# Performance work log

Hardware: AMD Instinct MI355X
Metric: run time of the kernel (lower is better)

## Reference

```python
import jax, jax.numpy as jnp
import numpy as np

EPS = 1e-6
K_HOPS = 2  # SGConv K


def setup_inputs() -> dict:
    key = jax.random.key(0)
    k1, k2, k3, k4 = jax.random.split(key, 4)
    B, Kk, C, T = 32, 8, 64, 250
    E, H = 4096, 128
    x = jax.random.normal(k1, (B, Kk, C, T), dtype=jnp.float32)
    edge_index = jax.random.randint(k2, (2, E), 0, C, dtype=jnp.int64)
    edge_weights = jax.random.uniform(k3, (E,), dtype=jnp.float32)
    W = jax.random.normal(k4, (H, Kk * T), dtype=jnp.float32) * 0.02
    b = jnp.zeros((H,), dtype=jnp.float32)
    return {"x": x, "edge_index": edge_index, "edge_weights": edge_weights, "W": W, "b": b}


def reference(x, edge_index, edge_weights, W, b):
    B, Kk, C, T = x.shape
    N = C  # nodes
    x = x.reshape(B, N, Kk * T)  # (B, N, F)

    # clamp non-positive edge weights to epsilon (mirrors in-place .data clamp)
    w = jnp.where(edge_weights <= 0, EPS, edge_weights)

    # gcn_norm with self loops (fill value 1.0)
    src, dst = edge_index[0], edge_index[1]
    loop = jnp.arange(N, dtype=edge_index.dtype)
    src = jnp.concatenate([src, loop])
    dst = jnp.concatenate([dst, loop])
    w = jnp.concatenate([w, jnp.ones((N,), w.dtype)])
    deg = jnp.zeros((N,), w.dtype).at[dst].add(w)
    dinv = jnp.where(deg > 0, deg ** -0.5, jnp.zeros_like(deg))
    norm = dinv[src] * w * dinv[dst]  # (E+N,)

    # K hops of gather -> weight -> scatter-add aggregation
    for _ in range(K_HOPS):
        msg = x[:, src, :] * norm[None, :, None]        # (B, E+N, F)
        x = jnp.zeros_like(x).at[:, dst, :].add(msg)    # (B, N, F)

    # final linear: y = x @ W^T + b
    return jnp.einsum('bnf,hf->bnh', x, W) + b
```

## Files before the change

kernel.cpp:

```cpp
#include <hip/hip_runtime.h>
#include <hip/hip_bf16.h>

#define EPSW 1e-6f

typedef __attribute__((ext_vector_type(4))) float floatx4;
typedef __attribute__((ext_vector_type(8))) short shortx8;

__device__ __forceinline__ unsigned short f2bf(float f) {
    unsigned int u = __float_as_uint(f);
    u = (u + 0x7fffu + ((u >> 16) & 1u)) >> 16;
    return (unsigned short)u;
}

__global__ __launch_bounds__(256) void prep(const float* __restrict__ x,
                                            const float* __restrict__ W,
                                            const int* __restrict__ ei,
                                            const float* __restrict__ ew,
                                            unsigned short* __restrict__ xt,
                                            unsigned short* __restrict__ wt,
                                            float* __restrict__ Mt) {
    __shared__ __align__(16) unsigned char smem[64 * 264 * 2];
    const int bid = blockIdx.x;
    const int t   = threadIdx.x;

    if (bid < 256) {
        unsigned short(*tile)[264] = (unsigned short(*)[264])smem;
        const int rb   = (bid >> 3) * 64;
        const int kgb  = (bid & 7) * 32;
        const int kbas = kgb * 8;
#pragma unroll
        for (int i = 0; i < 16; ++i) {
            const int idx = i * 256 + t;
            const int r   = idx >> 6;
            const int kc  = (idx & 63) * 4;
            const int k   = kbas + kc;
            floatx4 v = (floatx4){0.f, 0.f, 0.f, 0.f};
            if (k < 2000)
                v = *(const floatx4*)(x + (size_t)(rb + r) * 2000 + k);
            tile[r][kc + 0] = f2bf(v.x);
            tile[r][kc + 1] = f2bf(v.y);
            tile[r][kc + 2] = f2bf(v.z);
            tile[r][kc + 3] = f2bf(v.w);
        }
        __syncthreads();
#pragma unroll
        for (int i = 0; i < 8; ++i) {
            const int kg_l = i * 4 + (t >> 6);
            const int r    = t & 63;
            const shortx8 g = *(const shortx8*)&tile[r][kg_l * 8];
            *(shortx8*)(xt + ((size_t)(kgb + kg_l) * 2048 + rb + r) * 8) = g;
        }
    } else if (bid < 272) {
#pragma unroll
        for (int i = 0; i < 8; ++i) {
            const int G  = (bid - 256) * 2048 + i * 256 + t;
            const int kg = G >> 7;
            const int h  = G & 127;
            const int k  = kg * 8;
            floatx4 v0 = (floatx4){0.f, 0.f, 0.f, 0.f};
            floatx4 v1 = (floatx4){0.f, 0.f, 0.f, 0.f};
            if (k < 2000) {
                v0 = *(const floatx4*)(W + (size_t)h * 2000 + k);
                v1 = *(const floatx4*)(W + (size_t)h * 2000 + k + 4);
            }
            unsigned short* p = wt + ((size_t)kg * 128 + h) * 8;
            p[0] = f2bf(v0.x); p[1] = f2bf(v0.y); p[2] = f2bf(v0.z); p[3] = f2bf(v0.w);
            p[4] = f2bf(v1.x); p[5] = f2bf(v1.y); p[6] = f2bf(v1.z); p[7] = f2bf(v1.w);
        }
    } else {
        float* A    = (float*)smem;
        float* deg  = (float*)(smem + 16384);
        float* dinv = deg + 64;
        if (t < 64) deg[t] = 1.0f;
        for (int i = t; i < 4096; i += 256) A[i] = 0.0f;
        __syncthreads();
        const int* src = ei;
        const int* dst = ei + 4096;
        for (int e = t; e < 4096; e += 256) {
            float w = ew[e];
            w = (w <= 0.0f) ? EPSW : w;
            atomicAdd(&deg[dst[e]], w);
        }
        __syncthreads();
        if (t < 64) dinv[t] = 1.0f / sqrtf(deg[t]);
        __syncthreads();
        for (int e = t; e < 4096; e += 256) {
            float w = ew[e];
            w = (w <= 0.0f) ? EPSW : w;
            const int s = src[e], d = dst[e];
            atomicAdd(&A[d * 64 + s], dinv[s] * w * dinv[d]);
        }
        if (t < 64) atomicAdd(&A[t * 64 + t], dinv[t] * dinv[t]);
        __syncthreads();
#pragma unroll
        for (int i = 0; i < 16; ++i) {
            const int idx = i * 256 + t;
            const int n = idx >> 6, c = idx & 63;
            float s = 0.0f;
#pragma unroll 8
            for (int k = 0; k < 64; ++k) s += A[n * 64 + k] * A[k * 64 + c];
            Mt[c * 64 + n] = s;
        }
    }
}

__global__ __launch_bounds__(512) void gemm_apply(
        const unsigned short* __restrict__ xt,
        const unsigned short* __restrict__ wt,
        const float* __restrict__ Mt,
        const float* __restrict__ bias,
        float* __restrict__ y) {
    __shared__ float Ms[4096];
    __shared__ float zs[64][17];
    const int t    = threadIdx.x;
    const int wave = t >> 6, lane = t & 63;
    const int m = lane & 15, q = lane >> 4;
    const int ht = blockIdx.x;
    const int b  = blockIdx.y;
    const int rt = wave & 3, kh = wave >> 2;

    {
        const floatx4* Mg4 = (const floatx4*)Mt;
        floatx4* Ms4 = (floatx4*)Ms;
        Ms4[t]       = Mg4[t];
        Ms4[t + 512] = Mg4[t + 512];
    }

    const shortx8* Ag = (const shortx8*)xt;
    const shortx8* Bg = (const shortx8*)wt;
    int ga = (kh * 128 + q) * 2048 + b * 64 + rt * 16 + m;
    int gb = (kh * 128 + q) * 128 + ht * 16 + m;

    floatx4 acc0 = (floatx4){0.f, 0.f, 0.f, 0.f};
    floatx4 acc1 = (floatx4){0.f, 0.f, 0.f, 0.f};
#pragma unroll 4
    for (int kt = 0; kt < 32; kt += 2) {
        const shortx8 a0 = Ag[ga];
        const shortx8 b0 = Bg[gb];
        const shortx8 a1 = Ag[ga + 8192];
        const shortx8 b1 = Bg[gb + 512];
        acc0 = __builtin_amdgcn_mfma_f32_16x16x32_bf16(a0, b0, acc0, 0, 0, 0);
        acc1 = __builtin_amdgcn_mfma_f32_16x16x32_bf16(a1, b1, acc1, 0, 0, 0);
        ga += 16384; gb += 1024;
    }
    acc0 += acc1;

    __syncthreads();
    if (kh == 0) {
#pragma unroll
        for (int v = 0; v < 4; ++v) zs[rt * 16 + q * 4 + v][m] = acc0[v];
    }
    __syncthreads();
    if (kh == 1) {
#pragma unroll
        for (int v = 0; v < 4; ++v) zs[rt * 16 + q * 4 + v][m] += acc0[v];
    }
    __syncthreads();

    {
        const int n0 = t >> 4;
        const int h  = t & 15;
        const float bv = bias[ht * 16 + h];
        float s0 = bv, s1 = bv;
#pragma unroll
        for (int mm = 0; mm < 64; ++mm) {
            const float zv = zs[mm][h];
            s0 += Ms[mm * 64 + n0]      * zv;
            s1 += Ms[mm * 64 + n0 + 32] * zv;
        }
        float* yp = y + (size_t)b * 8192 + ht * 16 + h;
        yp[(size_t)n0 * 128]        = s0;
        yp[(size_t)(n0 + 32) * 128] = s1;
    }
}

extern "C" void kernel_launch(void* const* d_in, const int* in_sizes, int n_in,
                              void* d_out, int out_size, void* d_ws, size_t ws_size,
                              hipStream_t stream) {
    const float* x    = (const float*)d_in[0];
    const int*   ei   = (const int*)d_in[1];
    const float* ew   = (const float*)d_in[2];
    const float* W    = (const float*)d_in[3];
    const float* bias = (const float*)d_in[4];
    float* y = (float*)d_out;

    float* Mt = (float*)d_ws;
    unsigned short* xt = (unsigned short*)(Mt + 4096);
    unsigned short* wt = xt + 4194304;

    prep<<<273, 256, 0, stream>>>(x, W, ei, ew, xt, wt, Mt);
    gemm_apply<<<dim3(8, 32), 512, 0, stream>>>(xt, wt, Mt, bias, y);
}
```

Before: 102.5 us.

## Fuse prep and GEMM kernels into one launch with global counter spin-waits

Merges the bf16 conversion/transposition, graph-propagation matrix build and GEMM-apply kernels into a single 256-block kernel. Cross-block dependencies are handled with atomic counters in the workspace and spin-waits with sleep. The propagation matrix is computed by 16 blocks in parallel, and its wait is deferred until after the MFMA loop so that work can overlap. This removes a kernel launch and its boundary, but it needs all blocks to be co-resident. It also assumes the counter memory starts at either 0 or a 0xAA fill pattern, and the counters are never reset between calls.

```diff
diff --git a/kernel.cpp b/kernel.cpp
--- a/kernel.cpp
+++ b/kernel.cpp
@@ -2,6 +2,7 @@
 #include <hip/hip_bf16.h>
 
 #define EPSW 1e-6f
+#define BASEP 0xAAAAAAAAu
 
 typedef __attribute__((ext_vector_type(4))) float floatx4;
 typedef __attribute__((ext_vector_type(8))) short shortx8;
@@ -12,25 +13,34 @@
     return (unsigned short)u;
 }
 
-__global__ __launch_bounds__(256) void prep(const float* __restrict__ x,
-                                            const float* __restrict__ W,
-                                            const int* __restrict__ ei,
-                                            const float* __restrict__ ew,
-                                            unsigned short* __restrict__ xt,
-                                            unsigned short* __restrict__ wt,
-                                            float* __restrict__ Mt) {
-    __shared__ __align__(16) unsigned char smem[64 * 264 * 2];
+__device__ __forceinline__ void spin_until(const unsigned int* p, unsigned int tgt) {
+    for (int i = 0; i < 1000000; ++i) {
+        const unsigned int v =
+            __hip_atomic_load(p, __ATOMIC_RELAXED, __HIP_MEMORY_SCOPE_AGENT);
+        if (v == tgt || v == tgt + BASEP) return;
+        __builtin_amdgcn_s_sleep(2);
+    }
+}
+
+__global__ __launch_bounds__(512, 2) void fused(
+        const float* __restrict__ x, const float* __restrict__ W,
+        const int* __restrict__ ei, const float* __restrict__ ew,
+        const float* __restrict__ bias,
+        unsigned short* __restrict__ xt, unsigned short* __restrict__ wt,
+        float* __restrict__ Mt, unsigned int* __restrict__ ctr,
+        float* __restrict__ y) {
+    __shared__ __align__(16) unsigned char smem[50688];
     const int bid = blockIdx.x;
     const int t   = threadIdx.x;
 
-    if (bid < 256) {
+    {
         unsigned short(*tile)[264] = (unsigned short(*)[264])smem;
         const int rb   = (bid >> 3) * 64;
         const int kgb  = (bid & 7) * 32;
         const int kbas = kgb * 8;
 #pragma unroll
-        for (int i = 0; i < 16; ++i) {
-            const int idx = i * 256 + t;
+        for (int i = 0; i < 8; ++i) {
+            const int idx = i * 512 + t;
             const int r   = idx >> 6;
             const int kc  = (idx & 63) * 4;
             const int k   = kbas + kc;
@@ -44,17 +54,19 @@
         }
         __syncthreads();
 #pragma unroll
-        for (int i = 0; i < 8; ++i) {
-            const int kg_l = i * 4 + (t >> 6);
+        for (int i = 0; i < 4; ++i) {
+            const int kg_l = i * 8 + (t >> 6);
             const int r    = t & 63;
             const shortx8 g = *(const shortx8*)&tile[r][kg_l * 8];
             *(shortx8*)(xt + ((size_t)(kgb + kg_l) * 2048 + rb + r) * 8) = g;
         }
-    } else if (bid < 272) {
-#pragma unroll
-        for (int i = 0; i < 8; ++i) {
-            const int G  = (bid - 256) * 2048 + i * 256 + t;
-            const int kg = G >> 7;
+    }
+
+    if (bid < 16) {
+#pragma unroll
+        for (int i = 0; i < 4; ++i) {
+            const int G  = i * 512 + t;
+            const int kg = bid * 16 + (G >> 7);
             const int h  = G & 127;
             const int k  = kg * 8;
             floatx4 v0 = (floatx4){0.f, 0.f, 0.f, 0.f};
@@ -67,64 +79,65 @@
             p[0] = f2bf(v0.x); p[1] = f2bf(v0.y); p[2] = f2bf(v0.z); p[3] = f2bf(v0.w);
             p[4] = f2bf(v1.x); p[5] = f2bf(v1.y); p[6] = f2bf(v1.z); p[7] = f2bf(v1.w);
         }
-    } else {
-        float* A    = (float*)smem;
-        float* deg  = (float*)(smem + 16384);
-        float* dinv = deg + 64;
+    }
+
+    __syncthreads();
+    __threadfence();
+    if (t == 0) {
+        atomicAdd(&ctr[bid >> 3], 1u);
+        if (bid < 16) atomicAdd(&ctr[32], 1u);
+    }
+
+    if (bid >= 240) {
+        float* A    = (float*)(smem + 33792);
+        float* deg  = (float*)(smem + 50176);
+        float* dinv = (float*)(smem + 50432);
         if (t < 64) deg[t] = 1.0f;
-        for (int i = t; i < 4096; i += 256) A[i] = 0.0f;
-        __syncthreads();
-        const int* src = ei;
-        const int* dst = ei + 4096;
-        for (int e = t; e < 4096; e += 256) {
+        for (int i = t; i < 4096; i += 512) A[i] = 0.0f;
+        __syncthreads();
+        const int* srcp = ei;
+        const int* dstp = ei + 4096;
+        for (int e = t; e < 4096; e += 512) {
             float w = ew[e];
             w = (w <= 0.0f) ? EPSW : w;
-            atomicAdd(&deg[dst[e]], w);
+            atomicAdd(&deg[dstp[e]], w);
         }
         __syncthreads();
         if (t < 64) dinv[t] = 1.0f / sqrtf(deg[t]);
         __syncthreads();
-        for (int e = t; e < 4096; e += 256) {
+        for (int e = t; e < 4096; e += 512) {
             float w = ew[e];
             w = (w <= 0.0f) ? EPSW : w;
-            const int s = src[e], d = dst[e];
+            const int s = srcp[e], d = dstp[e];
             atomicAdd(&A[d * 64 + s], dinv[s] * w * dinv[d]);
         }
         if (t < 64) atomicAdd(&A[t * 64 + t], dinv[t] * dinv[t]);
         __syncthreads();
-#pragma unroll
-        for (int i = 0; i < 16; ++i) {
-            const int idx = i * 256 + t;
-            const int n = idx >> 6, c = idx & 63;
+        if (t < 256) {
+            const int c = (bid - 240) * 4 + (t >> 6);
+            const int n = t & 63;
             float s = 0.0f;
 #pragma unroll 8
             for (int k = 0; k < 64; ++k) s += A[n * 64 + k] * A[k * 64 + c];
             Mt[c * 64 + n] = s;
         }
-    }
-}
-
-__global__ __launch_bounds__(512) void gemm_apply(
-        const unsigned short* __restrict__ xt,
-        const unsigned short* __restrict__ wt,
-        const float* __restrict__ Mt,
-        const float* __restrict__ bias,
-        float* __restrict__ y) {
-    __shared__ float Ms[4096];
-    __shared__ float zs[64][17];
-    const int t    = threadIdx.x;
+        __syncthreads();
+        __threadfence();
+        if (t == 0) atomicAdd(&ctr[33], 1u);
+    }
+
+    const int b  = bid >> 3;
+    const int ht = bid & 7;
+    if (t == 0) {
+        spin_until(&ctr[b], 8u);
+        spin_until(&ctr[32], 16u);
+    }
+    __syncthreads();
+    __threadfence();
+
     const int wave = t >> 6, lane = t & 63;
     const int m = lane & 15, q = lane >> 4;
-    const int ht = blockIdx.x;
-    const int b  = blockIdx.y;
     const int rt = wave & 3, kh = wave >> 2;
-
-    {
-        const floatx4* Mg4 = (const floatx4*)Mt;
-        floatx4* Ms4 = (floatx4*)Ms;
-        Ms4[t]       = Mg4[t];
-        Ms4[t + 512] = Mg4[t + 512];
-    }
 
     const shortx8* Ag = (const shortx8*)xt;
     const shortx8* Bg = (const shortx8*)wt;
@@ -145,7 +158,18 @@
     }
     acc0 += acc1;
 
-    __syncthreads();
+    if (t == 0) spin_until(&ctr[33], 16u);
+    __syncthreads();
+    __threadfence();
+
+    float* Ms      = (float*)smem;
+    float(*zs)[17] = (float(*)[17])(smem + 16384);
+    {
+        const floatx4* Mg4 = (const floatx4*)Mt;
+        floatx4* Ms4 = (floatx4*)Ms;
+        Ms4[t]       = Mg4[t];
+        Ms4[t + 512] = Mg4[t + 512];
+    }
     if (kh == 0) {
 #pragma unroll
         for (int v = 0; v < 4; ++v) zs[rt * 16 + q * 4 + v][m] = acc0[v];
@@ -156,7 +180,6 @@
         for (int v = 0; v < 4; ++v) zs[rt * 16 + q * 4 + v][m] += acc0[v];
     }
     __syncthreads();
-
     {
         const int n0 = t >> 4;
         const int h  = t & 15;
@@ -187,7 +210,7 @@
     float* Mt = (float*)d_ws;
     unsigned short* xt = (unsigned short*)(Mt + 4096);
     unsigned short* wt = xt + 4194304;
-
-    prep<<<273, 256, 0, stream>>>(x, W, ei, ew, xt, wt, Mt);
-    gemm_apply<<<dim3(8, 32), 512, 0, stream>>>(xt, wt, Mt, bias, y);
-}
+    unsigned int* ctr  = (unsigned int*)(wt + 262144);
+
+    fused<<<256, 512, 0, stream>>>(x, W, ei, ew, bias, xt, wt, Mt, ctr, y);
+}
```

Measured after the change: 212.6 us. +107.5%, slower.

## Fuse prep and GEMM into one kernel with in-block bf16 conversion and LDS staging

Applied to the files above, without the earlier changes.

Merges the conversion/propagation-matrix prep kernel and the GEMM-apply kernel into a single launch. Each block recomputes the 64x64 two-hop propagation matrix in LDS, then streams fp32 x and W chunks from global memory, converts them to bf16 in registers with a cheaper perm-based pack, and stages them in double-buffered LDS for MFMA. This removes the second launch and the global round trip through bf16 workspace copies. In exchange every block redundantly builds the graph matrix with atomics and an O(64^3) product, x is re-read by all 8 head tiles, and the rounding drops the round-to-even tie handling.

```diff
diff --git a/kernel.cpp b/kernel.cpp
--- a/kernel.cpp
+++ b/kernel.cpp
@@ -6,146 +6,134 @@
 typedef __attribute__((ext_vector_type(4))) float floatx4;
 typedef __attribute__((ext_vector_type(8))) short shortx8;
 
-__device__ __forceinline__ unsigned short f2bf(float f) {
-    unsigned int u = __float_as_uint(f);
-    u = (u + 0x7fffu + ((u >> 16) & 1u)) >> 16;
-    return (unsigned short)u;
+__device__ __forceinline__ shortx8 pack8(floatx4 a, floatx4 b) {
+    union { shortx8 v; unsigned int u[4]; } r;
+    const unsigned a0 = __float_as_uint(a.x) + 0x8000u, a1 = __float_as_uint(a.y) + 0x8000u;
+    const unsigned a2 = __float_as_uint(a.z) + 0x8000u, a3 = __float_as_uint(a.w) + 0x8000u;
+    const unsigned b0 = __float_as_uint(b.x) + 0x8000u, b1 = __float_as_uint(b.y) + 0x8000u;
+    const unsigned b2 = __float_as_uint(b.z) + 0x8000u, b3 = __float_as_uint(b.w) + 0x8000u;
+    r.u[0] = __builtin_amdgcn_perm(a1, a0, 0x07060302u);
+    r.u[1] = __builtin_amdgcn_perm(a3, a2, 0x07060302u);
+    r.u[2] = __builtin_amdgcn_perm(b1, b0, 0x07060302u);
+    r.u[3] = __builtin_amdgcn_perm(b3, b2, 0x07060302u);
+    return r.v;
 }
 
-__global__ __launch_bounds__(256) void prep(const float* __restrict__ x,
-                                            const float* __restrict__ W,
-                                            const int* __restrict__ ei,
-                                            const float* __restrict__ ew,
-                                            unsigned short* __restrict__ xt,
-                                            unsigned short* __restrict__ wt,
-                                            float* __restrict__ Mt) {
-    __shared__ __align__(16) unsigned char smem[64 * 264 * 2];
+#define XSTR 136
+
+__global__ __launch_bounds__(512, 2) void fused_all(
+        const float* __restrict__ x, const float* __restrict__ W,
+        const int* __restrict__ ei, const float* __restrict__ ew,
+        const float* __restrict__ bias, float* __restrict__ y) {
+    __shared__ __align__(16) unsigned short smem[29952];
+    unsigned short* xs0 = smem;
+    unsigned short* xs1 = smem + 8704;
+    unsigned short* ww0 = smem + 17408;
+    unsigned short* ww1 = smem + 19584;
+    float* Ms = (float*)(smem + 21760);
+    float* A    = (float*)smem;
+    float* deg  = (float*)xs1;
+    float* dinv = deg + 64;
+    float(*zs)[17] = (float(*)[17])smem;
+
+    const int t   = threadIdx.x;
     const int bid = blockIdx.x;
-    const int t   = threadIdx.x;
+    const int b   = bid & 31;
+    const int ht  = bid >> 5;
 
-    if (bid < 256) {
-        unsigned short(*tile)[264] = (unsigned short(*)[264])smem;
-        const int rb   = (bid >> 3) * 64;
-        const int kgb  = (bid & 7) * 32;
-        const int kbas = kgb * 8;
-#pragma unroll
-        for (int i = 0; i < 16; ++i) {
-            const int idx = i * 256 + t;
-            const int r   = idx >> 6;
-            const int kc  = (idx & 63) * 4;
-            const int k   = kbas + kc;
-            floatx4 v = (floatx4){0.f, 0.f, 0.f, 0.f};
-            if (k < 2000)
-                v = *(const floatx4*)(x + (size_t)(rb + r) * 2000 + k);
-            tile[r][kc + 0] = f2bf(v.x);
-            tile[r][kc + 1] = f2bf(v.y);
-            tile[r][kc + 2] = f2bf(v.z);
-            tile[r][kc + 3] = f2bf(v.w);
-        }
+    {
+        if (t < 64) deg[t] = 1.0f;
+        for (int i = t; i < 4096; i += 512) A[i] = 0.0f;
         __syncthreads();
+        const int* srcp = ei;
+        const int* dstp = ei + 4096;
 #pragma unroll
         for (int i = 0; i < 8; ++i) {
-            const int kg_l = i * 4 + (t >> 6);
-            const int r    = t & 63;
-            const shortx8 g = *(const shortx8*)&tile[r][kg_l * 8];
-            *(shortx8*)(xt + ((size_t)(kgb + kg_l) * 2048 + rb + r) * 8) = g;
-        }
-    } else if (bid < 272) {
-#pragma unroll
-        for (int i = 0; i < 8; ++i) {
-            const int G  = (bid - 256) * 2048 + i * 256 + t;
-            const int kg = G >> 7;
-            const int h  = G & 127;
-            const int k  = kg * 8;
-            floatx4 v0 = (floatx4){0.f, 0.f, 0.f, 0.f};
-            floatx4 v1 = (floatx4){0.f, 0.f, 0.f, 0.f};
-            if (k < 2000) {
-                v0 = *(const floatx4*)(W + (size_t)h * 2000 + k);
-                v1 = *(const floatx4*)(W + (size_t)h * 2000 + k + 4);
-            }
-            unsigned short* p = wt + ((size_t)kg * 128 + h) * 8;
-            p[0] = f2bf(v0.x); p[1] = f2bf(v0.y); p[2] = f2bf(v0.z); p[3] = f2bf(v0.w);
-            p[4] = f2bf(v1.x); p[5] = f2bf(v1.y); p[6] = f2bf(v1.z); p[7] = f2bf(v1.w);
-        }
-    } else {
-        float* A    = (float*)smem;
-        float* deg  = (float*)(smem + 16384);
-        float* dinv = deg + 64;
-        if (t < 64) deg[t] = 1.0f;
-        for (int i = t; i < 4096; i += 256) A[i] = 0.0f;
-        __syncthreads();
-        const int* src = ei;
-        const int* dst = ei + 4096;
-        for (int e = t; e < 4096; e += 256) {
+            const int e = i * 512 + t;
             float w = ew[e];
             w = (w <= 0.0f) ? EPSW : w;
-            atomicAdd(&deg[dst[e]], w);
+            atomicAdd(&deg[dstp[e]], w);
         }
         __syncthreads();
         if (t < 64) dinv[t] = 1.0f / sqrtf(deg[t]);
         __syncthreads();
-        for (int e = t; e < 4096; e += 256) {
+#pragma unroll
+        for (int i = 0; i < 8; ++i) {
+            const int e = i * 512 + t;
             float w = ew[e];
             w = (w <= 0.0f) ? EPSW : w;
-            const int s = src[e], d = dst[e];
+            const int s = srcp[e], d = dstp[e];
             atomicAdd(&A[d * 64 + s], dinv[s] * w * dinv[d]);
         }
         if (t < 64) atomicAdd(&A[t * 64 + t], dinv[t] * dinv[t]);
         __syncthreads();
 #pragma unroll
-        for (int i = 0; i < 16; ++i) {
-            const int idx = i * 256 + t;
+        for (int i = 0; i < 8; ++i) {
+            const int idx = i * 512 + t;
             const int n = idx >> 6, c = idx & 63;
             float s = 0.0f;
 #pragma unroll 8
             for (int k = 0; k < 64; ++k) s += A[n * 64 + k] * A[k * 64 + c];
-            Mt[c * 64 + n] = s;
+            Ms[c * 64 + n] = s;
         }
+        __syncthreads();
     }
-}
 
-__global__ __launch_bounds__(512) void gemm_apply(
-        const unsigned short* __restrict__ xt,
-        const unsigned short* __restrict__ wt,
-        const float* __restrict__ Mt,
-        const float* __restrict__ bias,
-        float* __restrict__ y) {
-    __shared__ float Ms[4096];
-    __shared__ float zs[64][17];
-    const int t    = threadIdx.x;
     const int wave = t >> 6, lane = t & 63;
     const int m = lane & 15, q = lane >> 4;
-    const int ht = blockIdx.x;
-    const int b  = blockIdx.y;
     const int rt = wave & 3, kh = wave >> 2;
 
-    {
-        const floatx4* Mg4 = (const floatx4*)Mt;
-        floatx4* Ms4 = (floatx4*)Ms;
-        Ms4[t]       = Mg4[t];
-        Ms4[t + 512] = Mg4[t + 512];
+    const float* xb = x + (size_t)b * 64 * 2000;
+    const float* Wb = W + (size_t)ht * 16 * 2000;
+
+    const int xr0 = t >> 4,         xk0 = (t & 15) * 8;
+    const int xr1 = (t + 512) >> 4, xk1 = xk0;
+    const int wr  = t >> 4,         wk  = (t & 15) * 8;
+
+    floatx4 px0a, px0b, px1a, px1b, pwa, pwb;
+    const floatx4 zero4 = (floatx4){0.f, 0.f, 0.f, 0.f};
+
+#define LOAD_CHUNK(kbase)                                                     \
+    {                                                                         \
+        const int k0 = (kbase) + xk0;                                         \
+        if (k0 < 2000) {                                                      \
+            px0a = *(const floatx4*)(xb + (size_t)xr0 * 2000 + k0);           \
+            px0b = *(const floatx4*)(xb + (size_t)xr0 * 2000 + k0 + 4);       \
+            px1a = *(const floatx4*)(xb + (size_t)xr1 * 2000 + k0);           \
+            px1b = *(const floatx4*)(xb + (size_t)xr1 * 2000 + k0 + 4);       \
+        } else { px0a = zero4; px0b = zero4; px1a = zero4; px1b = zero4; }    \
+        if (t < 256) {                                                        \
+            const int kw = (kbase) + wk;                                      \
+            if (kw < 2000) {                                                  \
+                pwa = *(const floatx4*)(Wb + (size_t)wr * 2000 + kw);         \
+                pwb = *(const floatx4*)(Wb + (size_t)wr * 2000 + kw + 4);     \
+            } else { pwa = zero4; pwb = zero4; }                              \
+        }                                                                     \
     }
 
-    const shortx8* Ag = (const shortx8*)xt;
-    const shortx8* Bg = (const shortx8*)wt;
-    int ga = (kh * 128 + q) * 2048 + b * 64 + rt * 16 + m;
-    int gb = (kh * 128 + q) * 128 + ht * 16 + m;
+    LOAD_CHUNK(0);
 
-    floatx4 acc0 = (floatx4){0.f, 0.f, 0.f, 0.f};
-    floatx4 acc1 = (floatx4){0.f, 0.f, 0.f, 0.f};
-#pragma unroll 4
-    for (int kt = 0; kt < 32; kt += 2) {
-        const shortx8 a0 = Ag[ga];
-        const shortx8 b0 = Bg[gb];
-        const shortx8 a1 = Ag[ga + 8192];
-        const shortx8 b1 = Bg[gb + 512];
+    floatx4 acc0 = zero4, acc1 = zero4;
+    for (int c = 0; c < 16; ++c) {
+        unsigned short* xsb = (c & 1) ? xs1 : xs0;
+        unsigned short* wwb = (c & 1) ? ww1 : ww0;
+        *(shortx8*)&xsb[xr0 * XSTR + xk0] = pack8(px0a, px0b);
+        *(shortx8*)&xsb[xr1 * XSTR + xk1] = pack8(px1a, px1b);
+        if (t < 256) *(shortx8*)&wwb[wr * XSTR + wk] = pack8(pwa, pwb);
+        __syncthreads();
+        if (c < 15) LOAD_CHUNK((c + 1) * 128);
+        const unsigned short* xrow = &xsb[(rt * 16 + m) * XSTR + kh * 64 + q * 8];
+        const unsigned short* wrow = &wwb[m * XSTR + kh * 64 + q * 8];
+        const shortx8 a0 = *(const shortx8*)xrow;
+        const shortx8 b0 = *(const shortx8*)wrow;
+        const shortx8 a1 = *(const shortx8*)(xrow + 32);
+        const shortx8 b1 = *(const shortx8*)(wrow + 32);
         acc0 = __builtin_amdgcn_mfma_f32_16x16x32_bf16(a0, b0, acc0, 0, 0, 0);
         acc1 = __builtin_amdgcn_mfma_f32_16x16x32_bf16(a1, b1, acc1, 0, 0, 0);
-        ga += 16384; gb += 1024;
+        __syncthreads();
     }
     acc0 += acc1;
 
-    __syncthreads();
     if (kh == 0) {
 #pragma unroll
         for (int v = 0; v < 4; ++v) zs[rt * 16 + q * 4 + v][m] = acc0[v];
@@ -156,7 +144,6 @@
         for (int v = 0; v < 4; ++v) zs[rt * 16 + q * 4 + v][m] += acc0[v];
     }
     __syncthreads();
-
     {
         const int n0 = t >> 4;
         const int h  = t & 15;
@@ -184,10 +171,5 @@
     const float* bias = (const float*)d_in[4];
     float* y = (float*)d_out;
 
-    float* Mt = (float*)d_ws;
-    unsigned short* xt = (unsigned short*)(Mt + 4096);
-    unsigned short* wt = xt + 4194304;
-
-    prep<<<273, 256, 0, stream>>>(x, W, ei, ew, xt, wt, Mt);
-    gemm_apply<<<dim3(8, 32), 512, 0, stream>>>(xt, wt, Mt, bias, y);
+    fused_all<<<256, 512, 0, stream>>>(x, W, ei, ew, bias, y);
 }
```

Result: no change. 102.5 us (+0.0%).

## Read fp32 x directly in GEMM, dropping the bf16 transpose pass

Applied to the files above, without the earlier changes.

The separate prep pass that converted x to a transposed bf16 layout in workspace is gone. The GEMM now loads fp32 rows of x directly and packs them to bf16 in registers with a perm-based rounding, which removes one full write and re-read of the activation tensor. The graph matrix squaring is spread across 16 blocks that each redo the adjacency build, and GEMM blocks are ordered batch-fastest so blocks sharing W run together. Costs: the A loads are strided per lane and less coalesced, and the new rounding is round-half-up rather than round-to-nearest-even.

```diff
diff --git a/kernel.cpp b/kernel.cpp
--- a/kernel.cpp
+++ b/kernel.cpp
@@ -12,48 +12,30 @@
     return (unsigned short)u;
 }
 
-__global__ __launch_bounds__(256) void prep(const float* __restrict__ x,
-                                            const float* __restrict__ W,
+__device__ __forceinline__ shortx8 pack8(floatx4 a, floatx4 b) {
+    union { shortx8 v; unsigned int u[4]; } r;
+    const unsigned a0 = __float_as_uint(a.x) + 0x8000u, a1 = __float_as_uint(a.y) + 0x8000u;
+    const unsigned a2 = __float_as_uint(a.z) + 0x8000u, a3 = __float_as_uint(a.w) + 0x8000u;
+    const unsigned b0 = __float_as_uint(b.x) + 0x8000u, b1 = __float_as_uint(b.y) + 0x8000u;
+    const unsigned b2 = __float_as_uint(b.z) + 0x8000u, b3 = __float_as_uint(b.w) + 0x8000u;
+    r.u[0] = __builtin_amdgcn_perm(a1, a0, 0x07060302u);
+    r.u[1] = __builtin_amdgcn_perm(a3, a2, 0x07060302u);
+    r.u[2] = __builtin_amdgcn_perm(b1, b0, 0x07060302u);
+    r.u[3] = __builtin_amdgcn_perm(b3, b2, 0x07060302u);
+    return r.v;
+}
+
+__global__ __launch_bounds__(256) void prep(const float* __restrict__ W,
                                             const int* __restrict__ ei,
                                             const float* __restrict__ ew,
-                                            unsigned short* __restrict__ xt,
                                             unsigned short* __restrict__ wt,
                                             float* __restrict__ Mt) {
-    __shared__ __align__(16) unsigned char smem[64 * 264 * 2];
     const int bid = blockIdx.x;
     const int t   = threadIdx.x;
-
-    if (bid < 256) {
-        unsigned short(*tile)[264] = (unsigned short(*)[264])smem;
-        const int rb   = (bid >> 3) * 64;
-        const int kgb  = (bid & 7) * 32;
-        const int kbas = kgb * 8;
-#pragma unroll
-        for (int i = 0; i < 16; ++i) {
-            const int idx = i * 256 + t;
-            const int r   = idx >> 6;
-            const int kc  = (idx & 63) * 4;
-            const int k   = kbas + kc;
-            floatx4 v = (floatx4){0.f, 0.f, 0.f, 0.f};
-            if (k < 2000)
-                v = *(const floatx4*)(x + (size_t)(rb + r) * 2000 + k);
-            tile[r][kc + 0] = f2bf(v.x);
-            tile[r][kc + 1] = f2bf(v.y);
-            tile[r][kc + 2] = f2bf(v.z);
-            tile[r][kc + 3] = f2bf(v.w);
-        }
-        __syncthreads();
+    if (bid < 16) {
 #pragma unroll
         for (int i = 0; i < 8; ++i) {
-            const int kg_l = i * 4 + (t >> 6);
-            const int r    = t & 63;
-            const shortx8 g = *(const shortx8*)&tile[r][kg_l * 8];
-            *(shortx8*)(xt + ((size_t)(kgb + kg_l) * 2048 + rb + r) * 8) = g;
-        }
-    } else if (bid < 272) {
-#pragma unroll
-        for (int i = 0; i < 8; ++i) {
-            const int G  = (bid - 256) * 2048 + i * 256 + t;
+            const int G  = bid * 2048 + i * 256 + t;
             const int kg = G >> 7;
             const int h  = G & 127;
             const int k  = kg * 8;
@@ -68,44 +50,45 @@
             p[4] = f2bf(v1.x); p[5] = f2bf(v1.y); p[6] = f2bf(v1.z); p[7] = f2bf(v1.w);
         }
     } else {
-        float* A    = (float*)smem;
-        float* deg  = (float*)(smem + 16384);
-        float* dinv = deg + 64;
+        __shared__ float A[4096];
+        __shared__ float deg[64];
+        __shared__ float dinv[64];
         if (t < 64) deg[t] = 1.0f;
         for (int i = t; i < 4096; i += 256) A[i] = 0.0f;
         __syncthreads();
-        const int* src = ei;
-        const int* dst = ei + 4096;
-        for (int e = t; e < 4096; e += 256) {
+        const int* srcp = ei;
+        const int* dstp = ei + 4096;
+#pragma unroll
+        for (int i = 0; i < 16; ++i) {
+            const int e = i * 256 + t;
             float w = ew[e];
             w = (w <= 0.0f) ? EPSW : w;
-            atomicAdd(&deg[dst[e]], w);
+            atomicAdd(&deg[dstp[e]], w);
         }
         __syncthreads();
         if (t < 64) dinv[t] = 1.0f / sqrtf(deg[t]);
         __syncthreads();
-        for (int e = t; e < 4096; e += 256) {
+#pragma unroll
+        for (int i = 0; i < 16; ++i) {
+            const int e = i * 256 + t;
             float w = ew[e];
             w = (w <= 0.0f) ? EPSW : w;
-            const int s = src[e], d = dst[e];
+            const int s = srcp[e], d = dstp[e];
             atomicAdd(&A[d * 64 + s], dinv[s] * w * dinv[d]);
         }
         if (t < 64) atomicAdd(&A[t * 64 + t], dinv[t] * dinv[t]);
         __syncthreads();
-#pragma unroll
-        for (int i = 0; i < 16; ++i) {
-            const int idx = i * 256 + t;
-            const int n = idx >> 6, c = idx & 63;
-            float s = 0.0f;
+        const int c = (bid - 16) * 4 + (t >> 6);
+        const int n = t & 63;
+        float s = 0.0f;
 #pragma unroll 8
-            for (int k = 0; k < 64; ++k) s += A[n * 64 + k] * A[k * 64 + c];
-            Mt[c * 64 + n] = s;
-        }
+        for (int k = 0; k < 64; ++k) s += A[n * 64 + k] * A[k * 64 + c];
+        Mt[c * 64 + n] = s;
     }
 }
 
 __global__ __launch_bounds__(512) void gemm_apply(
-        const unsigned short* __restrict__ xt,
+        const float* __restrict__ x,
         const unsigned short* __restrict__ wt,
         const float* __restrict__ Mt,
         const float* __restrict__ bias,
@@ -113,10 +96,11 @@
     __shared__ float Ms[4096];
     __shared__ float zs[64][17];
     const int t    = threadIdx.x;
+    const int bid  = blockIdx.x;
+    const int b    = bid & 31;
+    const int ht   = bid >> 5;
     const int wave = t >> 6, lane = t & 63;
     const int m = lane & 15, q = lane >> 4;
-    const int ht = blockIdx.x;
-    const int b  = blockIdx.y;
     const int rt = wave & 3, kh = wave >> 2;
 
     {
@@ -126,26 +110,28 @@
         Ms4[t + 512] = Mg4[t + 512];
     }
 
-    const shortx8* Ag = (const shortx8*)xt;
+    const float* xrow = x + (size_t)(b * 64 + rt * 16 + m) * 2000;
+    const int kbase = kh * 1024 + q * 8;
     const shortx8* Bg = (const shortx8*)wt;
-    int ga = (kh * 128 + q) * 2048 + b * 64 + rt * 16 + m;
-    int gb = (kh * 128 + q) * 128 + ht * 16 + m;
+    const int gb = (kh * 128 + q) * 128 + ht * 16 + m;
 
-    floatx4 acc0 = (floatx4){0.f, 0.f, 0.f, 0.f};
-    floatx4 acc1 = (floatx4){0.f, 0.f, 0.f, 0.f};
-#pragma unroll 4
-    for (int kt = 0; kt < 32; kt += 2) {
-        const shortx8 a0 = Ag[ga];
-        const shortx8 b0 = Bg[gb];
-        const shortx8 a1 = Ag[ga + 8192];
-        const shortx8 b1 = Bg[gb + 512];
-        acc0 = __builtin_amdgcn_mfma_f32_16x16x32_bf16(a0, b0, acc0, 0, 0, 0);
-        acc1 = __builtin_amdgcn_mfma_f32_16x16x32_bf16(a1, b1, acc1, 0, 0, 0);
-        ga += 16384; gb += 1024;
+    const floatx4 zero4 = (floatx4){0.f, 0.f, 0.f, 0.f};
+    floatx4 acc0 = zero4, acc1 = zero4;
+#pragma unroll 8
+    for (int s = 0; s < 32; ++s) {
+        const int k0 = kbase + s * 32;
+        floatx4 f0 = zero4, f1 = zero4;
+        if (k0 < 2000) {
+            f0 = *(const floatx4*)(xrow + k0);
+            f1 = *(const floatx4*)(xrow + k0 + 4);
+        }
+        const shortx8 af = pack8(f0, f1);
+        const shortx8 bf = Bg[gb + s * 512];
+        if (s & 1) acc1 = __builtin_amdgcn_mfma_f32_16x16x32_bf16(af, bf, acc1, 0, 0, 0);
+        else       acc0 = __builtin_amdgcn_mfma_f32_16x16x32_bf16(af, bf, acc0, 0, 0, 0);
     }
     acc0 += acc1;
 
-    __syncthreads();
     if (kh == 0) {
 #pragma unroll
         for (int v = 0; v < 4; ++v) zs[rt * 16 + q * 4 + v][m] = acc0[v];
@@ -156,7 +142,6 @@
         for (int v = 0; v < 4; ++v) zs[rt * 16 + q * 4 + v][m] += acc0[v];
     }
     __syncthreads();
-
     {
         const int n0 = t >> 4;
         const int h  = t & 15;
@@ -185,9 +170,8 @@
     float* y = (float*)d_out;
 
     float* Mt = (float*)d_ws;
-    unsigned short* xt = (unsigned short*)(Mt + 4096);
-    unsigned short* wt = xt + 4194304;
+    unsigned short* wt = (unsigned short*)(Mt + 4096);
 
-    prep<<<273, 256, 0, stream>>>(x, W, ei, ew, xt, wt, Mt);
-    gemm_apply<<<dim3(8, 32), 512, 0, stream>>>(xt, wt, Mt, bias, y);
+    prep<<<32, 256, 0, stream>>>(W, ei, ew, wt, Mt);
+    gemm_apply<<<256, 512, 0, stream>>>(x, wt, Mt, bias, y);
 }
```

Result: faster. 97.91 us (-4.4%).
